# Optimization experiments

Hardware: AMD Instinct MI355X
Metric: run time of the kernel (lower is better)

Reference implementation:

```python
import jax, jax.numpy as jnp
import numpy as np

N, E, C, L, H = 32768, 524288, 128, 3, 4
B, S = 64, 512            # graphs, nodes per graph (N = B*S, equal-size graphs)
F_X, F_PE = 64, 16
IN_DIM = F_X + F_PE
HID, OUT = 256, 1
EPS = 1e-5                # BatchNorm1d eps
HD = C // H               # head dim


def setup_inputs():
    key = jax.random.key(0)
    ks = iter(jax.random.split(key, 32))
    rn = lambda shape, s=0.05: jax.random.normal(next(ks), shape, dtype=jnp.float32) * s
    return dict(
        x=jax.random.normal(next(ks), (N, F_X), dtype=jnp.float32),
        pe=jax.random.normal(next(ks), (N, F_PE), dtype=jnp.float32),
        edge_index=jax.random.randint(next(ks), (2, E), 0, N),
        batch=jnp.repeat(jnp.arange(B), S),
        W_emb=rn((IN_DIM, C)), b_emb=jnp.zeros((C,), jnp.float32),
        gcn_w=rn((L, C, C)), gcn_b=jnp.zeros((L, C), jnp.float32),
        in_w=rn((L, 3 * C, C)), in_b=jnp.zeros((L, 3 * C), jnp.float32),
        out_w=rn((L, C, C)), out_b=jnp.zeros((L, C), jnp.float32),
        mlp_w1=rn((L, C, 2 * C)), mlp_b1=jnp.zeros((L, 2 * C), jnp.float32),
        mlp_w2=rn((L, 2 * C, C)), mlp_b2=jnp.zeros((L, C), jnp.float32),
        g1=jnp.ones((L, C), jnp.float32), be1=jnp.zeros((L, C), jnp.float32),
        g2=jnp.ones((L, C), jnp.float32), be2=jnp.zeros((L, C), jnp.float32),
        g3=jnp.ones((L, C), jnp.float32), be3=jnp.zeros((L, C), jnp.float32),
        W_hid=rn((C, HID)), b_hid=jnp.zeros((HID,), jnp.float32),
        W_out=rn((HID, OUT)), b_out=jnp.zeros((OUT,), jnp.float32),
    )


def _bn(h, g, b):
    # BatchNorm1d over nodes (training-mode batch stats, biased var)
    mu = h.mean(0)
    var = h.var(0)
    return (h - mu) * jax.lax.rsqrt(var + EPS) * g + b


def _gelu(x):
    return jax.nn.gelu(x, approximate=False)  # torch F.gelu default is erf


def reference(x, pe, edge_index, batch, W_emb, b_emb, gcn_w, gcn_b, in_w, in_b,
              out_w, out_b, mlp_w1, mlp_b1, mlp_w2, mlp_b2, g1, be1, g2, be2,
              g3, be3, W_hid, b_hid, W_out, b_out):
    # GCN normalization with self-loops (computed once; topology fixed)
    loops = jnp.arange(N)
    src = jnp.concatenate([edge_index[0], loops])
    dst = jnp.concatenate([edge_index[1], loops])
    deg = jax.ops.segment_sum(jnp.ones_like(src, jnp.float32), dst, num_segments=N)
    dinv = jnp.where(deg > 0, jax.lax.rsqrt(deg), 0.0)
    coef = (dinv[src] * dinv[dst])[:, None]

    h = jnp.concatenate([x, pe], axis=-1) @ W_emb + b_emb  # [N,C]
    scale = jnp.asarray(1.0 / np.sqrt(HD), jnp.float32)

    for l in range(L):
        # --- local GCNConv + residual + BN ---
        xw = h @ gcn_w[l]
        loc = jax.ops.segment_sum(xw[src] * coef, dst, num_segments=N) + gcn_b[l]
        h1 = _bn(loc + h, g1[l], be1[l])
        # --- global multihead attention on dense batch [B,S,C] ---
        hd = h.reshape(B, S, C)
        qkv = hd @ in_w[l].T + in_b[l]
        q, k, v = jnp.split(qkv, 3, axis=-1)
        sh = lambda t: t.reshape(B, S, H, HD).transpose(0, 2, 1, 3)  # [B,H,S,HD]
        q, k, v = sh(q), sh(k), sh(v)
        att = jax.nn.softmax(jnp.einsum('bhqd,bhkd->bhqk', q, k) * scale, axis=-1)
        ao = jnp.einsum('bhqk,bhkd->bhqd', att, v).transpose(0, 2, 1, 3).reshape(N, C)
        ao = ao @ out_w[l].T + out_b[l]
        h2 = _bn(ao + h, g2[l], be2[l])
        # --- combine + MLP residual + BN, then outer GELU ---
        out = h1 + h2
        m = jax.nn.relu(out @ mlp_w1[l] + mlp_b1[l]) @ mlp_w2[l] + mlp_b2[l]
        h = _gelu(_bn(out + m, g3[l], be3[l]))

    # global mean pool over graphs
    cnt = jax.ops.segment_sum(jnp.ones((N,), jnp.float32), batch, num_segments=B)
    pooled = jax.ops.segment_sum(h, batch, num_segments=B) / cnt[:, None]
    z = _gelu(pooled @ W_hid + b_hid)
    return (z @ W_out + b_out).squeeze()  # [B]
```

## Files before the change

kernel.cpp:

```cpp
#include <hip/hip_runtime.h>
#include <hip/hip_bf16.h>
#include <math.h>

#define NNODES 32768
#define NEDGES 524288
#define CCH 128
#define NLAYERS 3
#define NHEADS 4
#define HDIM 32
#define NB_GRAPH 64
#define SNODES 512
#define INDIM 80
#define HIDDEN 256
#define BNEPS 1e-5f
#define ATTNSCALE 0.17677669529663689f

typedef _Float16 f16;
typedef f16 half8_t __attribute__((ext_vector_type(8)));
typedef f16 half4_t __attribute__((ext_vector_type(4)));
typedef float float4_t __attribute__((ext_vector_type(4)));

__device__ __forceinline__ float gelu_f(float x) {
    return 0.5f * x * (1.0f + erff(x * 0.70710678118654752f));
}

__global__ void k_count(const int* __restrict__ dst, int* __restrict__ deg) {
    int e = blockIdx.x * blockDim.x + threadIdx.x;
    if (e < NEDGES) atomicAdd(&deg[dst[e]], 1);
}

__global__ void k_dinv_from_deg(const int* __restrict__ deg, float* __restrict__ dinv) {
    int i = blockIdx.x * blockDim.x + threadIdx.x;
    if (i < NNODES) dinv[i] = rsqrtf((float)(deg[i] + 1));
}

__global__ __launch_bounds__(1024) void k_scan(const int* __restrict__ deg,
                                               int* __restrict__ rowptr,
                                               int* __restrict__ cursor) {
    __shared__ int sa[1024], sb[1024];
    int t = threadIdx.x;
    int base = t * 32;
    int local[32];
    int s = 0;
    #pragma unroll
    for (int i = 0; i < 32; i++) { local[i] = s; s += deg[base + i]; }
    sa[t] = s;
    __syncthreads();
    int* sp = sa; int* dp = sb;
    for (int off = 1; off < 1024; off <<= 1) {
        dp[t] = (t >= off) ? sp[t] + sp[t - off] : sp[t];
        __syncthreads();
        int* tmp = sp; sp = dp; dp = tmp;
    }
    int excl = (t == 0) ? 0 : sp[t - 1];
    #pragma unroll
    for (int i = 0; i < 32; i++) {
        int v = excl + local[i];
        rowptr[base + i] = v;
        cursor[base + i] = v;
    }
    if (t == 1023) rowptr[NNODES] = sp[1023];
}

__global__ void k_fill_edges(const int* __restrict__ src, const int* __restrict__ dst,
                             int* __restrict__ cursor, int* __restrict__ col) {
    int e = blockIdx.x * blockDim.x + threadIdx.x;
    if (e >= NEDGES) return;
    int pos = atomicAdd(&cursor[dst[e]], 1);
    col[pos] = src[e];
}

__global__ void k_concat(const float* __restrict__ x, const float* __restrict__ pe,
                         float* __restrict__ out) {
    int gid = blockIdx.x * blockDim.x + threadIdx.x;
    if (gid >= NNODES * 32) return;
    int n = gid >> 5, q = gid & 31;
    float4 v = {0.f, 0.f, 0.f, 0.f};
    if (q < 16)      v = ((const float4*)x)[(size_t)n * 16 + q];
    else if (q < 20) v = ((const float4*)pe)[(size_t)n * 4 + (q - 16)];
    ((float4*)out)[gid] = v;
}

__global__ void k_wconv(const float* __restrict__ src, f16* __restrict__ hi,
                        f16* __restrict__ lo, int Nn, int Ks, int Kp, int trans,
                        int L, int ostride) {
    int gid = blockIdx.x * blockDim.x + threadIdx.x;
    int per = Nn * Kp;
    if (gid >= per * L) return;
    int l = gid / per, r = gid % per;
    int n = r / Kp, k = r % Kp;
    float v = 0.f;
    if (k < Ks)
        v = trans ? src[(size_t)l * Nn * Ks + (size_t)n * Ks + k]
                  : src[(size_t)l * Ks * Nn + (size_t)k * Nn + n];
    f16 h = (f16)v;
    size_t o = (size_t)l * ostride + r;
    hi[o] = h;
    lo[o] = (f16)(v - (float)h);
}

template<int ACT, bool SPLIT>
__global__ __launch_bounds__(256) void k_gemm_mfma(
        const float* __restrict__ A, const f16* __restrict__ Whi,
        const f16* __restrict__ Wlo, const float* __restrict__ bias,
        const float* __restrict__ rowscale, float* __restrict__ C,
        int M, int N, int K, f16* __restrict__ C2h,
        const float* __restrict__ bias2, f16* __restrict__ Cf16) {
    __shared__ f16 Ah[128 * 40];
    __shared__ f16 Al[128 * 40];
    __shared__ f16 Bh[128 * 40];
    __shared__ f16 Bl[128 * 40];
    const int t = threadIdx.x;
    const int bm = blockIdx.y * 128, bn = blockIdx.x * 128;
    const int w = t >> 6, lane = t & 63;
    const int g = lane >> 4, q = lane & 15;

    float4_t acc[2][8];
    #pragma unroll
    for (int mt = 0; mt < 2; mt++)
        #pragma unroll
        for (int nt = 0; nt < 8; nt++)
            acc[mt][nt] = (float4_t){0.f, 0.f, 0.f, 0.f};

    const int srow = t >> 1, shf = (t & 1) * 16;

    for (int kc = 0; kc < K; kc += 32) {
        {
            const float* ap = A + (size_t)(bm + srow) * K + kc + shf;
            float va[16];
            *(float4*)&va[0]  = ((const float4*)ap)[0];
            *(float4*)&va[4]  = ((const float4*)ap)[1];
            *(float4*)&va[8]  = ((const float4*)ap)[2];
            *(float4*)&va[12] = ((const float4*)ap)[3];
            half8_t h0, h1, l0, l1;
            #pragma unroll
            for (int j = 0; j < 8; j++) {
                f16 h = (f16)va[j];
                h0[j] = h; l0[j] = (f16)(va[j] - (float)h);
            }
            #pragma unroll
            for (int j = 0; j < 8; j++) {
                f16 h = (f16)va[8 + j];
                h1[j] = h; l1[j] = (f16)(va[8 + j] - (float)h);
            }
            *(half8_t*)&Ah[srow * 40 + shf]     = h0;
            *(half8_t*)&Ah[srow * 40 + shf + 8] = h1;
            *(half8_t*)&Al[srow * 40 + shf]     = l0;
            *(half8_t*)&Al[srow * 40 + shf + 8] = l1;
        }
        {
            const f16* bp = Whi + (size_t)(bn + srow) * K + kc + shf;
            *(half8_t*)&Bh[srow * 40 + shf]     = ((const half8_t*)bp)[0];
            *(half8_t*)&Bh[srow * 40 + shf + 8] = ((const half8_t*)bp)[1];
            const f16* lp = Wlo + (size_t)(bn + srow) * K + kc + shf;
            *(half8_t*)&Bl[srow * 40 + shf]     = ((const half8_t*)lp)[0];
            *(half8_t*)&Bl[srow * 40 + shf + 8] = ((const half8_t*)lp)[1];
        }
        __syncthreads();

        half8_t ah[2], al[2];
        #pragma unroll
        for (int mt = 0; mt < 2; mt++) {
            ah[mt] = *(half8_t*)&Ah[(w * 32 + mt * 16 + q) * 40 + g * 8];
            al[mt] = *(half8_t*)&Al[(w * 32 + mt * 16 + q) * 40 + g * 8];
        }
        #pragma unroll
        for (int nt = 0; nt < 8; nt++) {
            half8_t bh = *(half8_t*)&Bh[(nt * 16 + q) * 40 + g * 8];
            half8_t bl = *(half8_t*)&Bl[(nt * 16 + q) * 40 + g * 8];
            #pragma unroll
            for (int mt = 0; mt < 2; mt++) {
                acc[mt][nt] = __builtin_amdgcn_mfma_f32_16x16x32_f16(ah[mt], bh, acc[mt][nt], 0, 0, 0);
                acc[mt][nt] = __builtin_amdgcn_mfma_f32_16x16x32_f16(al[mt], bh, acc[mt][nt], 0, 0, 0);
                acc[mt][nt] = __builtin_amdgcn_mfma_f32_16x16x32_f16(ah[mt], bl, acc[mt][nt], 0, 0, 0);
            }
        }
        __syncthreads();
    }

    #pragma unroll
    for (int mt = 0; mt < 2; mt++) {
        #pragma unroll
        for (int r = 0; r < 4; r++) {
            int row = bm + w * 32 + mt * 16 + 4 * g + r;
            if constexpr (SPLIT) {
                if (blockIdx.x == 0) {
                    float rs = rowscale[row];
                    #pragma unroll
                    for (int nt = 0; nt < 8; nt++) {
                        int cn = bn + nt * 16 + q;
                        Cf16[(size_t)row * 128 + cn] = (f16)(acc[mt][nt][r] * rs);
                    }
                } else {
                    float ksc = (blockIdx.x == 2) ? ATTNSCALE : 1.0f;
                    #pragma unroll
                    for (int nt = 0; nt < 8; nt++) {
                        int cn2 = bn - 128 + nt * 16 + q;
                        C2h[(size_t)row * 384 + cn2] =
                            (f16)((acc[mt][nt][r] + bias2[cn2]) * ksc);
                    }
                }
            } else {
                float rs = rowscale ? rowscale[row] : 1.0f;
                #pragma unroll
                for (int nt = 0; nt < 8; nt++) {
                    int cn = bn + nt * 16 + q;
                    float v = acc[mt][nt][r] + (bias ? bias[cn] : 0.0f);
                    v *= rs;
                    if (ACT == 1) v = fmaxf(v, 0.0f);
                    C[(size_t)row * N + cn] = v;
                }
            }
        }
    }
}

__global__ __launch_bounds__(256) void k_gcn_gather_f16(
        const int* __restrict__ rowptr, const int* __restrict__ col,
        const f16* __restrict__ xws, const float* __restrict__ dinv,
        const float* __restrict__ bias, float* __restrict__ loc) {
    int t = threadIdx.x;
    int node = blockIdx.x * 16 + (t >> 4);
    int q = t & 15;
    int r0 = rowptr[node], r1 = rowptr[node + 1];
    half8_t sv = ((const half8_t*)(xws + (size_t)node * CCH))[q];
    float acc[8];
    #pragma unroll
    for (int i = 0; i < 8; i++) acc[i] = (float)sv[i];
    for (int j = r0; j < r1; j++) {
        int s = col[j];
        half8_t v = ((const half8_t*)(xws + (size_t)s * CCH))[q];
        #pragma unroll
        for (int i = 0; i < 8; i++) acc[i] += (float)v[i];
    }
    float dv = dinv[node];
    float4 b0 = ((const float4*)bias)[2 * q];
    float4 b1 = ((const float4*)bias)[2 * q + 1];
    float4 o0, o1;
    o0.x = fmaf(acc[0], dv, b0.x); o0.y = fmaf(acc[1], dv, b0.y);
    o0.z = fmaf(acc[2], dv, b0.z); o0.w = fmaf(acc[3], dv, b0.w);
    o1.x = fmaf(acc[4], dv, b1.x); o1.y = fmaf(acc[5], dv, b1.y);
    o1.z = fmaf(acc[6], dv, b1.z); o1.w = fmaf(acc[7], dv, b1.w);
    float* lp = loc + (size_t)node * CCH + q * 8;
    ((float4*)lp)[0] = o0;
    ((float4*)lp)[1] = o1;
}

__global__ __launch_bounds__(256) void k_bn_stats(const float* __restrict__ a,
                                                  const float* __restrict__ b,
                                                  float* __restrict__ part) {
    __shared__ float s1[256], s2[256];
    int t = threadIdx.x, blk = blockIdx.x;
    int c = t & 127, half = t >> 7;
    float sum = 0.f, sq = 0.f;
    for (int i = 0; i < 128; i++) {
        size_t r = (size_t)blk * 256 + half + 2 * i;
        float v = a[r * CCH + c] + b[r * CCH + c];
        sum += v;
        sq = fmaf(v, v, sq);
    }
    s1[t] = sum; s2[t] = sq;
    __syncthreads();
    if (t < 128) {
        part[blk * 256 + t]       = s1[t] + s1[t + 128];
        part[blk * 256 + 128 + t] = s2[t] + s2[t + 128];
    }
}

__global__ __launch_bounds__(1024) void k_bn_finalize(const float* __restrict__ part,
                                                      const float* __restrict__ g,
                                                      const float* __restrict__ be,
                                                      float* __restrict__ sc,
                                                      float* __restrict__ sh) {
    __shared__ float rs_[1024], rq_[1024];
    int t = threadIdx.x;
    int c = t & 127, sl = t >> 7;
    float s = 0.f, sq = 0.f;
    for (int bk = sl; bk < 128; bk += 8) {
        s  += part[bk * 256 + c];
        sq += part[bk * 256 + 128 + c];
    }
    rs_[sl * 128 + c] = s;
    rq_[sl * 128 + c] = sq;
    __syncthreads();
    if (t < 128) {
        float ss = 0.f, qq = 0.f;
        #pragma unroll
        for (int k = 0; k < 8; k++) { ss += rs_[k * 128 + t]; qq += rq_[k * 128 + t]; }
        float mu = ss / (float)NNODES;
        float var = qq / (float)NNODES - mu * mu;
        float rsv = rsqrtf(var + BNEPS);
        float gg = g[t] * rsv;
        sc[t] = gg;
        sh[t] = be[t] - mu * gg;
    }
}

template<int ACT>
__global__ void k_bn_apply(const float* __restrict__ a, const float* __restrict__ b,
                           const float* __restrict__ sc, const float* __restrict__ sh,
                           float* __restrict__ out) {
    int gid = blockIdx.x * blockDim.x + threadIdx.x;
    if (gid >= NNODES * 32) return;
    int c = (gid & 31) * 4;
    float4 av = ((const float4*)a)[gid];
    float4 bv = ((const float4*)b)[gid];
    float r[4];
    float xs[4] = {av.x + bv.x, av.y + bv.y, av.z + bv.z, av.w + bv.w};
    #pragma unroll
    for (int j = 0; j < 4; j++) {
        float v = fmaf(xs[j], sc[c + j], sh[c + j]);
        if (ACT == 2) v = gelu_f(v);
        r[j] = v;
    }
    float4 o = {r[0], r[1], r[2], r[3]};
    ((float4*)out)[gid] = o;
}

__global__ void k_bn_apply_add(const float* __restrict__ a, const float* __restrict__ b,
                               const float* __restrict__ sc, const float* __restrict__ sh,
                               float* __restrict__ io) {
    int gid = blockIdx.x * blockDim.x + threadIdx.x;
    if (gid >= NNODES * 32) return;
    int c = (gid & 31) * 4;
    float4 av = ((const float4*)a)[gid];
    float4 bv = ((const float4*)b)[gid];
    float4 ov = ((const float4*)io)[gid];
    float xs[4] = {av.x + bv.x, av.y + bv.y, av.z + bv.z, av.w + bv.w};
    float r[4] = {ov.x, ov.y, ov.z, ov.w};
    #pragma unroll
    for (int j = 0; j < 4; j++) r[j] += fmaf(xs[j], sc[c + j], sh[c + j]);
    float4 o = {r[0], r[1], r[2], r[3]};
    ((float4*)io)[gid] = o;
}

__global__ __launch_bounds__(512) void k_attn_flash(const f16* __restrict__ qkv,
                                                    float* __restrict__ ao) {
    __shared__ f16 Ks[512 * 40];
    __shared__ f16 VT[32 * 512];
    const int bh = blockIdx.x;
    const int b = bh >> 2, hh = bh & 3;
    const int t = threadIdx.x;
    const int lane = t & 63, wave = t >> 6;
    const int g = lane >> 4, q16 = lane & 15;

    const f16* base = qkv + (size_t)b * SNODES * 384;

    #pragma unroll
    for (int it = 0; it < 4; it++) {
        int u = it * 512 + t;
        int row = u >> 2, c = u & 3;
        half8_t hv = *(const half8_t*)(base + (size_t)row * 384 + CCH + hh * HDIM + c * 8);
        *(half8_t*)(Ks + row * 40 + c * 8) = hv;
    }

    #pragma unroll
    for (int it = 0; it < 8; it++) {
        int j4 = (t >> 3) & 3;
        int n  = it * 64 + ((t >> 5) & 15) * 4 + j4;
        int c  = t & 7;
        half4_t hv = *(const half4_t*)(base + (size_t)n * 384 + 2 * CCH + hh * HDIM + c * 4);
        float4 v = {(float)hv[0], (float)hv[1], (float)hv[2], (float)hv[3]};
        float4 u1;
        u1.x = __shfl_xor(v.x, 8); u1.y = __shfl_xor(v.y, 8);
        u1.z = __shfl_xor(v.z, 8); u1.w = __shfl_xor(v.w, 8);
        float4 w;
        if ((t & 8) == 0) { w.x = v.x;  w.y = u1.x; w.z = v.z;  w.w = u1.z; }
        else              { w.x = u1.y; w.y = v.y;  w.z = u1.w; w.w = v.w;  }
        float4 u2;
        u2.x = __shfl_xor(w.x, 16); u2.y = __shfl_xor(w.y, 16);
        u2.z = __shfl_xor(w.z, 16); u2.w = __shfl_xor(w.w, 16);
        float4 o;
        if ((t & 16) == 0) { o.x = w.x;  o.y = w.y;  o.z = u2.x; o.w = u2.y; }
        else               { o.x = u2.z; o.y = u2.w; o.z = w.z;  o.w = w.w;  }
        int hd = c * 4 + j4;
        int n0 = it * 64 + ((t >> 5) & 15) * 4;
        half4_t pk;
        pk[0] = (f16)o.x; pk[1] = (f16)o.y; pk[2] = (f16)o.z; pk[3] = (f16)o.w;
        int pos = ((n0 >> 2) + hd) & 127;
        *(half4_t*)(VT + hd * 512 + pos * 4) = pk;
    }
    __syncthreads();

    for (int j = 0; j < 4; j++) {
        int qt = wave * 4 + j;

        half8_t qf = *(const half8_t*)(base + (size_t)(qt * 16 + q16) * 384 + hh * HDIM + g * 8);

        float m = -1e30f, l = 0.f;
        float4_t oa0 = {0.f, 0.f, 0.f, 0.f}, oa1 = {0.f, 0.f, 0.f, 0.f};

        for (int ci = 0; ci < 4; ci++) {
            float4_t acc[8];
            #pragma unroll
            for (int ktl = 0; ktl < 8; ktl++) {
                half8_t kf = *(half8_t*)(Ks + ((ci * 8 + ktl) * 16 + q16) * 40 + g * 8);
                float4_t z = {0.f, 0.f, 0.f, 0.f};
                acc[ktl] = __builtin_amdgcn_mfma_f32_16x16x32_f16(kf, qf, z, 0, 0, 0);
            }

            float cm = -1e30f;
            #pragma unroll
            for (int ktl = 0; ktl < 8; ktl++)
                cm = fmaxf(cm, fmaxf(fmaxf(acc[ktl][0], acc[ktl][1]),
                                     fmaxf(acc[ktl][2], acc[ktl][3])));
            cm = fmaxf(cm, __shfl_xor(cm, 16));
            cm = fmaxf(cm, __shfl_xor(cm, 32));

            float mn = fmaxf(m, cm);
            float scq = __expf(m - mn);
            m = mn;
            l *= scq;
            #pragma unroll
            for (int r = 0; r < 4; r++) {
                float scr = __shfl(scq, 4 * g + r);
                oa0[r] *= scr;
                oa1[r] *= scr;
            }

            half8_t pa[4];
            #pragma unroll
            for (int Tl = 0; Tl < 4; Tl++) {
                #pragma unroll
                for (int i = 0; i < 4; i++) {
                    float e0 = __expf(acc[2 * Tl][i] - m);
                    float e1 = __expf(acc[2 * Tl + 1][i] - m);
                    l += e0 + e1;
                    pa[Tl][i]     = (f16)e0;
                    pa[Tl][4 + i] = (f16)e1;
                }
            }

            #pragma unroll
            for (int Tl = 0; Tl < 4; Tl++) {
                int T = ci * 4 + Tl;
                int hd0 = q16;
                half4_t b00 = *(half4_t*)(VT + hd0 * 512 + (((8 * T + g + hd0) & 127) * 4));
                half4_t b01 = *(half4_t*)(VT + hd0 * 512 + (((8 * T + 4 + g + hd0) & 127) * 4));
                half8_t vb0;
                vb0[0] = b00[0]; vb0[1] = b00[1]; vb0[2] = b00[2]; vb0[3] = b00[3];
                vb0[4] = b01[0]; vb0[5] = b01[1]; vb0[6] = b01[2]; vb0[7] = b01[3];
                oa0 = __builtin_amdgcn_mfma_f32_16x16x32_f16(pa[Tl], vb0, oa0, 0, 0, 0);
                int hd1 = 16 + q16;
                half4_t b10 = *(half4_t*)(VT + hd1 * 512 + (((8 * T + g + hd1) & 127) * 4));
                half4_t b11 = *(half4_t*)(VT + hd1 * 512 + (((8 * T + 4 + g + hd1) & 127) * 4));
                half8_t vb1;
                vb1[0] = b10[0]; vb1[1] = b10[1]; vb1[2] = b10[2]; vb1[3] = b10[3];
                vb1[4] = b11[0]; vb1[5] = b11[1]; vb1[6] = b11[2]; vb1[7] = b11[3];
                oa1 = __builtin_amdgcn_mfma_f32_16x16x32_f16(pa[Tl], vb1, oa1, 0, 0, 0);
            }
        }

        l += __shfl_xor(l, 16);
        l += __shfl_xor(l, 32);
        float invq = 1.0f / l;
        #pragma unroll
        for (int r = 0; r < 4; r++) {
            float invr = __shfl(invq, 4 * g + r);
            size_t row = (size_t)(b * SNODES + qt * 16 + 4 * g + r);
            ao[row * CCH + hh * HDIM + q16]      = oa0[r] * invr;
            ao[row * CCH + hh * HDIM + 16 + q16] = oa1[r] * invr;
        }
    }
}

__global__ __launch_bounds__(256) void k_pool2(const float* __restrict__ h,
                                               const int* __restrict__ batch,
                                               float* __restrict__ pooled,
                                               float* __restrict__ cnt) {
    __shared__ float bins[NB_GRAPH * 132];
    __shared__ int cbin[NB_GRAPH];
    int t = threadIdx.x;
    for (int i = t; i < NB_GRAPH * 132; i += 256) bins[i] = 0.f;
    if (t < NB_GRAPH) cbin[t] = 0;
    __syncthreads();
    int n0 = blockIdx.x * 256;
    int q = t & 31, ro = t >> 5;
    float4 racc = {0.f, 0.f, 0.f, 0.f};
    int ccount = 0;
    int gcur = batch[n0 + ro];
    for (int i = 0; i < 32; i++) {
        int n = n0 + i * 8 + ro;
        int g = batch[n];
        if (g != gcur) {
            atomicAdd(&bins[gcur * 132 + 4 * q + 0], racc.x);
            atomicAdd(&bins[gcur * 132 + 4 * q + 1], racc.y);
            atomicAdd(&bins[gcur * 132 + 4 * q + 2], racc.z);
            atomicAdd(&bins[gcur * 132 + 4 * q + 3], racc.w);
            if (q == 0) atomicAdd(&cbin[gcur], ccount);
            racc = (float4){0.f, 0.f, 0.f, 0.f};
            ccount = 0;
            gcur = g;
        }
        float4 v = ((const float4*)(h + (size_t)n * CCH))[q];
        racc.x += v.x; racc.y += v.y; racc.z += v.z; racc.w += v.w;
        ccount++;
    }
    atomicAdd(&bins[gcur * 132 + 4 * q + 0], racc.x);
    atomicAdd(&bins[gcur * 132 + 4 * q + 1], racc.y);
    atomicAdd(&bins[gcur * 132 + 4 * q + 2], racc.z);
    atomicAdd(&bins[gcur * 132 + 4 * q + 3], racc.w);
    if (q == 0) atomicAdd(&cbin[gcur], ccount);
    __syncthreads();
    for (int i = t; i < NB_GRAPH * CCH; i += 256) {
        int g = i >> 7, cc = i & 127;
        float v = bins[g * 132 + cc];
        if (v != 0.f) atomicAdd(&pooled[g * CCH + cc], v);
    }
    if (t < NB_GRAPH && cbin[t]) atomicAdd(&cnt[t], (float)cbin[t]);
}

__global__ __launch_bounds__(256) void k_head(const float* __restrict__ pooled,
                                              const float* __restrict__ cnt,
                                              const float* __restrict__ Wh,
                                              const float* __restrict__ bh,
                                              const float* __restrict__ Wo,
                                              const float* __restrict__ bo,
                                              float* __restrict__ out) {
    __shared__ float p[128];
    __shared__ float red[256];
    int g = blockIdx.x, t = threadIdx.x;
    if (t < 128) p[t] = pooled[g * CCH + t] / cnt[g];
    __syncthreads();
    float a = bh[t];
    for (int k = 0; k < 128; k++) a = fmaf(p[k], Wh[k * HIDDEN + t], a);
    float z = gelu_f(a);
    red[t] = z * Wo[t];
    __syncthreads();
    for (int s = 128; s > 0; s >>= 1) {
        if (t < s) red[t] += red[t + s];
        __syncthreads();
    }
    if (t == 0) out[g] = red[0] + bo[0];
}

extern "C" void kernel_launch(void* const* d_in, const int* in_sizes, int n_in,
                              void* d_out, int out_size, void* d_ws, size_t ws_size,
                              hipStream_t stream) {
    const float* x      = (const float*)d_in[0];
    const float* pe     = (const float*)d_in[1];
    const int*   ei     = (const int*)d_in[2];
    const int*   batch  = (const int*)d_in[3];
    const float* W_emb  = (const float*)d_in[4];
    const float* b_emb  = (const float*)d_in[5];
    const float* gcn_w  = (const float*)d_in[6];
    const float* gcn_b  = (const float*)d_in[7];
    const float* in_w   = (const float*)d_in[8];
    const float* in_b   = (const float*)d_in[9];
    const float* out_w  = (const float*)d_in[10];
    const float* out_b  = (const float*)d_in[11];
    const float* mlp_w1 = (const float*)d_in[12];
    const float* mlp_b1 = (const float*)d_in[13];
    const float* mlp_w2 = (const float*)d_in[14];
    const float* mlp_b2 = (const float*)d_in[15];
    const float* g1     = (const float*)d_in[16];
    const float* be1    = (const float*)d_in[17];
    const float* g2     = (const float*)d_in[18];
    const float* be2    = (const float*)d_in[19];
    const float* g3     = (const float*)d_in[20];
    const float* be3    = (const float*)d_in[21];
    const float* W_hid  = (const float*)d_in[22];
    const float* b_hid  = (const float*)d_in[23];
    const float* W_out  = (const float*)d_in[24];
    const float* b_out  = (const float*)d_in[25];
    float* out = (float*)d_out;

    float* ws = (float*)d_ws;
    const size_t NC = (size_t)NNODES * CCH;
    float* dinv   = ws;
    float* h      = dinv + NNODES;
    float* A      = h + NC;
    float* Bb     = A + NC;
    float* scr    = Bb + NC;
    float* part   = scr + (size_t)NNODES * 384;
    float* sc     = part + 128 * 256;
    float* sh     = sc + CCH;
    float* pooled = sh + CCH;
    float* cnt    = pooled + (size_t)NB_GRAPH * CCH;
    int*   ideg   = (int*)(cnt + NB_GRAPH);
    int*   rowptr = ideg + NNODES;
    int*   cursor = rowptr + NNODES + 1;
    int*   col    = cursor + NNODES;
    f16* wb    = (f16*)(col + NEDGES);
    f16* embh  = wb;                      f16* embl = embh + 128 * 128;
    f16* cwh   = embl + 128 * 128;        f16* cwl  = cwh + 3 * 512 * 128;
    f16* outh  = cwl + 3 * 512 * 128;     f16* outl = outh + 3 * 128 * 128;
    f16* m1h   = outl + 3 * 128 * 128;    f16* m1l  = m1h + 3 * 256 * 128;
    f16* m2h   = m1l + 3 * 256 * 128;     f16* m2l  = m2h + 3 * 128 * 256;
    f16* xws16 = m2l + 3 * 128 * 256;
    f16* qkv16 = xws16 + NC;

    const int* srcp = ei;
    const int* dstp = ei + NEDGES;

    const int NC4 = NNODES * 32;

    hipMemsetAsync(ideg, 0, NNODES * sizeof(int), stream);
    k_count<<<NEDGES / 256, 256, 0, stream>>>(dstp, ideg);
    k_dinv_from_deg<<<NNODES / 256, 256, 0, stream>>>(ideg, dinv);
    k_scan<<<1, 1024, 0, stream>>>(ideg, rowptr, cursor);
    k_fill_edges<<<NEDGES / 256, 256, 0, stream>>>(srcp, dstp, cursor, col);

    k_wconv<<<(128 * 128 + 255) / 256, 256, 0, stream>>>(W_emb, embh, embl, 128, 80, 128, 0, 1, 128 * 128);
    k_wconv<<<(3 * 128 * 128 + 255) / 256, 256, 0, stream>>>(gcn_w, cwh, cwl, 128, 128, 128, 0, 3, 512 * 128);
    k_wconv<<<(3 * 384 * 128 + 255) / 256, 256, 0, stream>>>(in_w, cwh + 128 * 128, cwl + 128 * 128, 384, 128, 128, 1, 3, 512 * 128);
    k_wconv<<<(3 * 128 * 128 + 255) / 256, 256, 0, stream>>>(out_w, outh, outl, 128, 128, 128, 1, 3, 128 * 128);
    k_wconv<<<(3 * 256 * 128 + 255) / 256, 256, 0, stream>>>(mlp_w1, m1h, m1l, 256, 128, 128, 0, 3, 256 * 128);
    k_wconv<<<(3 * 128 * 256 + 255) / 256, 256, 0, stream>>>(mlp_w2, m2h, m2l, 128, 256, 256, 0, 3, 128 * 256);

    k_concat<<<NC4 / 256, 256, 0, stream>>>(x, pe, A);
    k_gemm_mfma<0, false><<<dim3(1, NNODES / 128), 256, 0, stream>>>(
        A, embh, embl, b_emb, nullptr, h, NNODES, CCH, 128, nullptr, nullptr, nullptr);

    for (int l = 0; l < NLAYERS; l++) {
        k_gemm_mfma<0, true><<<dim3(4, NNODES / 128), 256, 0, stream>>>(
            h, cwh + (size_t)l * 512 * 128, cwl + (size_t)l * 512 * 128,
            nullptr, dinv, nullptr, NNODES, 512, 128, qkv16, in_b + l * 384, xws16);
        k_gcn_gather_f16<<<NNODES / 16, 256, 0, stream>>>(
            rowptr, col, xws16, dinv, gcn_b + l * CCH, Bb);
        k_bn_stats<<<128, 256, 0, stream>>>(Bb, h, part);
        k_bn_finalize<<<1, 1024, 0, stream>>>(part, g1 + l * CCH, be1 + l * CCH, sc, sh);
        k_bn_apply<0><<<NC4 / 256, 256, 0, stream>>>(Bb, h, sc, sh, A);

        k_attn_flash<<<NB_GRAPH * NHEADS, 512, 0, stream>>>(qkv16, Bb);
        k_gemm_mfma<0, false><<<dim3(1, NNODES / 128), 256, 0, stream>>>(
            Bb, outh + (size_t)l * 128 * 128, outl + (size_t)l * 128 * 128,
            out_b + l * CCH, nullptr, scr, NNODES, CCH, 128, nullptr, nullptr, nullptr);
        k_bn_stats<<<128, 256, 0, stream>>>(scr, h, part);
        k_bn_finalize<<<1, 1024, 0, stream>>>(part, g2 + l * CCH, be2 + l * CCH, sc, sh);
        k_bn_apply_add<<<NC4 / 256, 256, 0, stream>>>(scr, h, sc, sh, A);

        k_gemm_mfma<1, false><<<dim3(2, NNODES / 128), 256, 0, stream>>>(
            A, m1h + (size_t)l * 256 * 128, m1l + (size_t)l * 256 * 128,
            mlp_b1 + l * 256, nullptr, scr, NNODES, 256, 128, nullptr, nullptr, nullptr);
        k_gemm_mfma<0, false><<<dim3(1, NNODES / 128), 256, 0, stream>>>(
            scr, m2h + (size_t)l * 128 * 256, m2l + (size_t)l * 128 * 256,
            mlp_b2 + l * CCH, nullptr, Bb, NNODES, CCH, 256, nullptr, nullptr, nullptr);
        k_bn_stats<<<128, 256, 0, stream>>>(A, Bb, part);
        k_bn_finalize<<<1, 1024, 0, stream>>>(part, g3 + l * CCH, be3 + l * CCH, sc, sh);
        k_bn_apply<2><<<NC4 / 256, 256, 0, stream>>>(A, Bb, sc, sh, h);
    }

    hipMemsetAsync(pooled, 0, ((size_t)NB_GRAPH * CCH + NB_GRAPH) * sizeof(float), stream);
    k_pool2<<<NNODES / 256, 256, 0, stream>>>(h, batch, pooled, cnt);
    k_head<<<NB_GRAPH, 256, 0, stream>>>(pooled, cnt, W_hid, b_hid, W_out, b_out, out);
}
```

Measured before the change: 815.4 us.

## Merge BN1/BN2 finalize and apply passes, fuse weight conversion and dinv launches

Defers the first BatchNorm apply until after attention so that both BN finalizes run in one kernel and both BN applies run in one elementwise pass, which writes A directly. This removes one full-tensor read/write pass and two launches per layer. It also folds the six weight-conversion launches into one and computes dinv inside the scan kernel, cutting launch overhead. Attention output now goes to A instead of Bb, and Bb keeps the GCN result alive longer, so buffer lifetimes must line up.

```diff
diff --git a/kernel.cpp b/kernel.cpp
--- a/kernel.cpp
+++ b/kernel.cpp
@@ -29,21 +29,21 @@
     if (e < NEDGES) atomicAdd(&deg[dst[e]], 1);
 }
 
-__global__ void k_dinv_from_deg(const int* __restrict__ deg, float* __restrict__ dinv) {
-    int i = blockIdx.x * blockDim.x + threadIdx.x;
-    if (i < NNODES) dinv[i] = rsqrtf((float)(deg[i] + 1));
-}
-
 __global__ __launch_bounds__(1024) void k_scan(const int* __restrict__ deg,
                                                int* __restrict__ rowptr,
-                                               int* __restrict__ cursor) {
+                                               int* __restrict__ cursor,
+                                               float* __restrict__ dinv) {
     __shared__ int sa[1024], sb[1024];
     int t = threadIdx.x;
     int base = t * 32;
     int local[32];
     int s = 0;
     #pragma unroll
-    for (int i = 0; i < 32; i++) { local[i] = s; s += deg[base + i]; }
+    for (int i = 0; i < 32; i++) {
+        int d = deg[base + i];
+        local[i] = s; s += d;
+        dinv[base + i] = rsqrtf((float)(d + 1));
+    }
     sa[t] = s;
     __syncthreads();
     int* sp = sa; int* dp = sb;
@@ -81,13 +81,12 @@
     ((float4*)out)[gid] = v;
 }
 
-__global__ void k_wconv(const float* __restrict__ src, f16* __restrict__ hi,
-                        f16* __restrict__ lo, int Nn, int Ks, int Kp, int trans,
-                        int L, int ostride) {
-    int gid = blockIdx.x * blockDim.x + threadIdx.x;
+__device__ __forceinline__ void wconv_one(const float* __restrict__ src,
+                                          f16* __restrict__ hi, f16* __restrict__ lo,
+                                          int idx, int Nn, int Ks, int Kp, int trans,
+                                          int ostride) {
     int per = Nn * Kp;
-    if (gid >= per * L) return;
-    int l = gid / per, r = gid % per;
+    int l = idx / per, r = idx % per;
     int n = r / Kp, k = r % Kp;
     float v = 0.f;
     if (k < Ks)
@@ -97,6 +96,28 @@
     size_t o = (size_t)l * ostride + r;
     hi[o] = h;
     lo[o] = (f16)(v - (float)h);
+}
+
+__global__ void k_wconv_all(const float* __restrict__ W_emb, const float* __restrict__ gcn_w,
+                            const float* __restrict__ in_w, const float* __restrict__ out_w,
+                            const float* __restrict__ m1, const float* __restrict__ m2,
+                            f16* embh, f16* embl, f16* cwh, f16* cwl,
+                            f16* outh, f16* outl, f16* m1h, f16* m1l,
+                            f16* m2h, f16* m2l) {
+    int gid = blockIdx.x * blockDim.x + threadIdx.x;
+    if (gid < 16384) {
+        wconv_one(W_emb, embh, embl, gid, 128, 80, 128, 0, 128 * 128);
+    } else if (gid < 65536) {
+        wconv_one(gcn_w, cwh, cwl, gid - 16384, 128, 128, 128, 0, 512 * 128);
+    } else if (gid < 212992) {
+        wconv_one(in_w, cwh + 128 * 128, cwl + 128 * 128, gid - 65536, 384, 128, 128, 1, 512 * 128);
+    } else if (gid < 262144) {
+        wconv_one(out_w, outh, outl, gid - 212992, 128, 128, 128, 1, 128 * 128);
+    } else if (gid < 360448) {
+        wconv_one(m1, m1h, m1l, gid - 262144, 256, 128, 128, 0, 256 * 128);
+    } else if (gid < 458752) {
+        wconv_one(m2, m2h, m2l, gid - 360448, 128, 256, 256, 0, 128 * 256);
+    }
 }
 
 template<int ACT, bool SPLIT>
@@ -296,6 +317,39 @@
     }
 }
 
+__global__ __launch_bounds__(1024) void k_bn_finalize2(
+        const float* __restrict__ part1, const float* __restrict__ part2,
+        const float* __restrict__ g1, const float* __restrict__ be1,
+        const float* __restrict__ g2, const float* __restrict__ be2,
+        float* __restrict__ sc1, float* __restrict__ sh1,
+        float* __restrict__ sc2, float* __restrict__ sh2) {
+    __shared__ float rs_[1024], rq_[1024];
+    int t = threadIdx.x;
+    int c = t & 127, sl = t >> 7;
+    const float* p = (sl < 4) ? part1 : part2;
+    int s0 = sl & 3;
+    float s = 0.f, sq = 0.f;
+    for (int bk = s0; bk < 128; bk += 4) {
+        s  += p[bk * 256 + c];
+        sq += p[bk * 256 + 128 + c];
+    }
+    rs_[sl * 128 + c] = s;
+    rq_[sl * 128 + c] = sq;
+    __syncthreads();
+    if (t < 256) {
+        int which = t >> 7, cc = t & 127;
+        int o = which * 512;
+        float ss = 0.f, qq = 0.f;
+        #pragma unroll
+        for (int k = 0; k < 4; k++) { ss += rs_[o + k * 128 + cc]; qq += rq_[o + k * 128 + cc]; }
+        float mu = ss / (float)NNODES;
+        float var = qq / (float)NNODES - mu * mu;
+        float rsv = rsqrtf(var + BNEPS);
+        if (which == 0) { float gg = g1[cc] * rsv; sc1[cc] = gg; sh1[cc] = be1[cc] - mu * gg; }
+        else            { float gg = g2[cc] * rsv; sc2[cc] = gg; sh2[cc] = be2[cc] - mu * gg; }
+    }
+}
+
 template<int ACT>
 __global__ void k_bn_apply(const float* __restrict__ a, const float* __restrict__ b,
                            const float* __restrict__ sc, const float* __restrict__ sh,
@@ -317,21 +371,29 @@
     ((float4*)out)[gid] = o;
 }
 
-__global__ void k_bn_apply_add(const float* __restrict__ a, const float* __restrict__ b,
-                               const float* __restrict__ sc, const float* __restrict__ sh,
-                               float* __restrict__ io) {
+__global__ void k_bn_apply2(const float* __restrict__ Bb, const float* __restrict__ h,
+                            const float* __restrict__ scr,
+                            const float* __restrict__ sc1, const float* __restrict__ sh1,
+                            const float* __restrict__ sc2, const float* __restrict__ sh2,
+                            float* __restrict__ A) {
     int gid = blockIdx.x * blockDim.x + threadIdx.x;
     if (gid >= NNODES * 32) return;
     int c = (gid & 31) * 4;
-    float4 av = ((const float4*)a)[gid];
-    float4 bv = ((const float4*)b)[gid];
-    float4 ov = ((const float4*)io)[gid];
-    float xs[4] = {av.x + bv.x, av.y + bv.y, av.z + bv.z, av.w + bv.w};
-    float r[4] = {ov.x, ov.y, ov.z, ov.w};
-    #pragma unroll
-    for (int j = 0; j < 4; j++) r[j] += fmaf(xs[j], sc[c + j], sh[c + j]);
+    float4 bv = ((const float4*)Bb)[gid];
+    float4 hv = ((const float4*)h)[gid];
+    float4 sv = ((const float4*)scr)[gid];
+    float b4[4] = {bv.x, bv.y, bv.z, bv.w};
+    float h4[4] = {hv.x, hv.y, hv.z, hv.w};
+    float s4[4] = {sv.x, sv.y, sv.z, sv.w};
+    float r[4];
+    #pragma unroll
+    for (int j = 0; j < 4; j++) {
+        float x1 = b4[j] + h4[j];
+        float x2 = s4[j] + h4[j];
+        r[j] = fmaf(x1, sc1[c + j], sh1[c + j]) + fmaf(x2, sc2[c + j], sh2[c + j]);
+    }
     float4 o = {r[0], r[1], r[2], r[3]};
-    ((float4*)io)[gid] = o;
+    ((float4*)A)[gid] = o;
 }
 
 __global__ __launch_bounds__(512) void k_attn_flash(const f16* __restrict__ qkv,
@@ -413,9 +475,9 @@
             l *= scq;
             #pragma unroll
             for (int r = 0; r < 4; r++) {
-                float scr = __shfl(scq, 4 * g + r);
-                oa0[r] *= scr;
-                oa1[r] *= scr;
+                float scr_ = __shfl(scq, 4 * g + r);
+                oa0[r] *= scr_;
+                oa1[r] *= scr_;
             }
 
             half8_t pa[4];
@@ -572,10 +634,13 @@
     float* A      = h + NC;
     float* Bb     = A + NC;
     float* scr    = Bb + NC;
-    float* part   = scr + (size_t)NNODES * 384;
-    float* sc     = part + 128 * 256;
-    float* sh     = sc + CCH;
-    float* pooled = sh + CCH;
+    float* part1  = scr + (size_t)NNODES * 384;
+    float* part2  = part1 + 128 * 256;
+    float* sc1    = part2 + 128 * 256;
+    float* sh1    = sc1 + CCH;
+    float* sc2    = sh1 + CCH;
+    float* sh2    = sc2 + CCH;
+    float* pooled = sh2 + CCH;
     float* cnt    = pooled + (size_t)NB_GRAPH * CCH;
     int*   ideg   = (int*)(cnt + NB_GRAPH);
     int*   rowptr = ideg + NNODES;
@@ -597,16 +662,12 @@
 
     hipMemsetAsync(ideg, 0, NNODES * sizeof(int), stream);
     k_count<<<NEDGES / 256, 256, 0, stream>>>(dstp, ideg);
-    k_dinv_from_deg<<<NNODES / 256, 256, 0, stream>>>(ideg, dinv);
-    k_scan<<<1, 1024, 0, stream>>>(ideg, rowptr, cursor);
+    k_scan<<<1, 1024, 0, stream>>>(ideg, rowptr, cursor, dinv);
     k_fill_edges<<<NEDGES / 256, 256, 0, stream>>>(srcp, dstp, cursor, col);
 
-    k_wconv<<<(128 * 128 + 255) / 256, 256, 0, stream>>>(W_emb, embh, embl, 128, 80, 128, 0, 1, 128 * 128);
-    k_wconv<<<(3 * 128 * 128 + 255) / 256, 256, 0, stream>>>(gcn_w, cwh, cwl, 128, 128, 128, 0, 3, 512 * 128);
-    k_wconv<<<(3 * 384 * 128 + 255) / 256, 256, 0, stream>>>(in_w, cwh + 128 * 128, cwl + 128 * 128, 384, 128, 128, 1, 3, 512 * 128);
-    k_wconv<<<(3 * 128 * 128 + 255) / 256, 256, 0, stream>>>(out_w, outh, outl, 128, 128, 128, 1, 3, 128 * 128);
-    k_wconv<<<(3 * 256 * 128 + 255) / 256, 256, 0, stream>>>(mlp_w1, m1h, m1l, 256, 128, 128, 0, 3, 256 * 128);
-    k_wconv<<<(3 * 128 * 256 + 255) / 256, 256, 0, stream>>>(mlp_w2, m2h, m2l, 128, 256, 256, 0, 3, 128 * 256);
+    k_wconv_all<<<458752 / 256, 256, 0, stream>>>(
+        W_emb, gcn_w, in_w, out_w, mlp_w1, mlp_w2,
+        embh, embl, cwh, cwl, outh, outl, m1h, m1l, m2h, m2l);
 
     k_concat<<<NC4 / 256, 256, 0, stream>>>(x, pe, A);
     k_gemm_mfma<0, false><<<dim3(1, NNODES / 128), 256, 0, stream>>>(
@@ -618,17 +679,17 @@
             nullptr, dinv, nullptr, NNODES, 512, 128, qkv16, in_b + l * 384, xws16);
         k_gcn_gather_f16<<<NNODES / 16, 256, 0, stream>>>(
             rowptr, col, xws16, dinv, gcn_b + l * CCH, Bb);
-        k_bn_stats<<<128, 256, 0, stream>>>(Bb, h, part);
-        k_bn_finalize<<<1, 1024, 0, stream>>>(part, g1 + l * CCH, be1 + l * CCH, sc, sh);
-        k_bn_apply<0><<<NC4 / 256, 256, 0, stream>>>(Bb, h, sc, sh, A);
-
-        k_attn_flash<<<NB_GRAPH * NHEADS, 512, 0, stream>>>(qkv16, Bb);
+        k_bn_stats<<<128, 256, 0, stream>>>(Bb, h, part1);
+
+        k_attn_flash<<<NB_GRAPH * NHEADS, 512, 0, stream>>>(qkv16, A);
         k_gemm_mfma<0, false><<<dim3(1, NNODES / 128), 256, 0, stream>>>(
-            Bb, outh + (size_t)l * 128 * 128, outl + (size_t)l * 128 * 128,
+            A, outh + (size_t)l * 128 * 128, outl + (size_t)l * 128 * 128,
             out_b + l * CCH, nullptr, scr, NNODES, CCH, 128, nullptr, nullptr, nullptr);
-        k_bn_stats<<<128, 256, 0, stream>>>(scr, h, part);
-        k_bn_finalize<<<1, 1024, 0, stream>>>(part, g2 + l * CCH, be2 + l * CCH, sc, sh);
-        k_bn_apply_add<<<NC4 / 256, 256, 0, stream>>>(scr, h, sc, sh, A);
+        k_bn_stats<<<128, 256, 0, stream>>>(scr, h, part2);
+        k_bn_finalize2<<<1, 1024, 0, stream>>>(part1, part2,
+            g1 + l * CCH, be1 + l * CCH, g2 + l * CCH, be2 + l * CCH,
+            sc1, sh1, sc2, sh2);
+        k_bn_apply2<<<NC4 / 256, 256, 0, stream>>>(Bb, h, scr, sc1, sh1, sc2, sh2, A);
 
         k_gemm_mfma<1, false><<<dim3(2, NNODES / 128), 256, 0, stream>>>(
             A, m1h + (size_t)l * 256 * 128, m1l + (size_t)l * 256 * 128,
@@ -636,9 +697,9 @@
         k_gemm_mfma<0, false><<<dim3(1, NNODES / 128), 256, 0, stream>>>(
             scr, m2h + (size_t)l * 128 * 256, m2l + (size_t)l * 128 * 256,
             mlp_b2 + l * CCH, nullptr, Bb, NNODES, CCH, 256, nullptr, nullptr, nullptr);
-        k_bn_stats<<<128, 256, 0, stream>>>(A, Bb, part);
-        k_bn_finalize<<<1, 1024, 0, stream>>>(part, g3 + l * CCH, be3 + l * CCH, sc, sh);
-        k_bn_apply<2><<<NC4 / 256, 256, 0, stream>>>(A, Bb, sc, sh, h);
+        k_bn_stats<<<128, 256, 0, stream>>>(A, Bb, part1);
+        k_bn_finalize<<<1, 1024, 0, stream>>>(part1, g3 + l * CCH, be3 + l * CCH, sc1, sh1);
+        k_bn_apply<2><<<NC4 / 256, 256, 0, stream>>>(A, Bb, sc1, sh1, h);
     }
 
     hipMemsetAsync(pooled, 0, ((size_t)NB_GRAPH * CCH + NB_GRAPH) * sizeof(float), stream);
```

After: 782.4 us. 1.04x faster.
